# Optimization experiments

Hardware: AMD Instinct MI355X
Metric: run time of the kernel (lower is better)

## Reference

```python
import jax, jax.numpy as jnp
import numpy as np

EPS = 1e-4
# 8 box corners as min/max selection bits (matches the torch cat order:
# mmm, mmx, mxm, mxx, xmm, xmx, xxm, xxx)
_BITS = jnp.array([[0,0,0],[0,0,1],[0,1,0],[0,1,1],[1,0,0],[1,0,1],[1,1,0],[1,1,1]], dtype=jnp.float32)


def setup_inputs() -> dict:
    key = jax.random.key(0)
    k1, k2, k3, k4, k5 = jax.random.split(key, 5)
    K = 1024
    bb_min = jax.random.uniform(k1, (K, 3), minval=-1.0, maxval=1.0)
    size = jax.random.uniform(k2, (K, 3), minval=0.05, maxval=0.4)
    bb_max = bb_min + size
    # well-conditioned affine transforms: near-identity linear block + translation
    R = jnp.eye(3, dtype=jnp.float32) + 0.1 * jax.random.normal(k3, (K, 3, 3))
    t = 0.5 * jax.random.normal(k4, (K, 3))
    top = jnp.concatenate([R, t[:, :, None]], axis=-1)            # [K,3,4]
    bottom = jnp.broadcast_to(jnp.array([[0.0, 0.0, 0.0, 1.0]], dtype=jnp.float32), (K, 1, 4))
    abs_transforms = jnp.concatenate([top, bottom], axis=1)       # [K,4,4]
    selfpen_disable_mat = jax.random.randint(k5, (K, K), 0, 2) > 0
    return {"bb_min": bb_min, "bb_max": bb_max,
            "abs_transforms": abs_transforms,
            "selfpen_disable_mat": selfpen_disable_mat}


def reference(bb_min, bb_max, abs_transforms, selfpen_disable_mat):
    K = bb_min.shape[0]
    bits = _BITS.astype(bb_min.dtype)
    # corners: [K,8,3]
    corners = bb_min[:, None, :] * (1.0 - bits) + bb_max[:, None, :] * bits
    hcorners = jnp.concatenate([corners, jnp.ones((K, 8, 1), dtype=bb_min.dtype)], axis=-1)  # [K,8,4]
    # pose each box's corners by its own transform
    hposed = jnp.einsum('kij,kcj->kci', abs_transforms, hcorners)  # [K,8,4]
    # project every posed corner into every box's local frame
    back_trans = jnp.linalg.inv(abs_transforms)                    # [K,4,4]
    proj = jnp.einsum('kij,lcj->klci', back_trans, hposed)[..., :3]  # [K,K,8,3]
    inside = ((proj > bb_min[:, None, None, :] + EPS)
              & (proj < bb_max[:, None, None, :] - EPS)).all(axis=-1).any(axis=-1)  # [K,K]
    inside = inside & selfpen_disable_mat
    inside = inside | inside.T
    inside = jnp.tril(inside)
    # fixed-size index extraction (pad with -1): equivalent of
    # torch.stack(torch.where(inside)).sort(dim=0)[0].t()
    rows, cols = jnp.nonzero(inside, size=K * K, fill_value=-1)
    inds = jnp.stack([jnp.minimum(rows, cols), jnp.maximum(rows, cols)], axis=-1)  # [K*K,2], padded with -1
    return hposed[..., :3], inds
```

## Files before the change

kernel.cpp:

```cpp
#include <hip/hip_runtime.h>
#include <stdint.h>

#define KBOX 1024
#define EPSF 1e-4f
#define SLACK 3e-5f
#define ACT_TILES 2560
#define POSE_BLOCKS 4

#define BM_OFF 0
#define TC_OFF 131072

__device__ inline void inv_affine(const float r[12], float* o) {
    double m00 = r[0], m01 = r[1], m02 = r[2];
    double m10 = r[4], m11 = r[5], m12 = r[6];
    double m20 = r[8], m21 = r[9], m22 = r[10];
    double c00 = m11 * m22 - m12 * m21;
    double c01 = m12 * m20 - m10 * m22;
    double c02 = m10 * m21 - m11 * m20;
    double det = m00 * c00 + m01 * c01 + m02 * c02;
    double id = 1.0 / det;
    double i00 = c00 * id, i01 = (m02 * m21 - m01 * m22) * id, i02 = (m01 * m12 - m02 * m11) * id;
    double i10 = c01 * id, i11 = (m00 * m22 - m02 * m20) * id, i12 = (m02 * m10 - m00 * m12) * id;
    double i20 = c02 * id, i21 = (m01 * m20 - m00 * m21) * id, i22 = (m00 * m11 - m01 * m10) * id;
    double tx = r[3], ty = r[7], tz = r[11];
    o[0] = (float)i00; o[1] = (float)i01; o[2] = (float)i02;
    o[3] = (float)(-(i00 * tx + i01 * ty + i02 * tz));
    o[4] = (float)i10; o[5] = (float)i11; o[6] = (float)i12;
    o[7] = (float)(-(i10 * tx + i11 * ty + i12 * tz));
    o[8] = (float)i20; o[9] = (float)i21; o[10] = (float)i22;
    o[11] = (float)(-(i20 * tx + i21 * ty + i22 * tz));
}

__global__ void k_main(const float* __restrict__ bbmin, const float* __restrict__ bbmax,
                       const float* __restrict__ A, const uint8_t* __restrict__ disB,
                       float* __restrict__ out_hposed,
                       uint64_t* __restrict__ bm, uint32_t* __restrict__ tileCnt) {
    int bid = blockIdx.x;
    int t = threadIdx.x;

    if (bid >= ACT_TILES) {
        int k = (bid - ACT_TILES) * 256 + t;
        float r[12];
#pragma unroll
        for (int i = 0; i < 3; ++i) {
            float4 a4 = *(const float4*)(A + (size_t)k * 16 + i * 4);
            r[i * 4 + 0] = a4.x; r[i * 4 + 1] = a4.y; r[i * 4 + 2] = a4.z; r[i * 4 + 3] = a4.w;
        }
        float bmn[3], bmx[3];
#pragma unroll
        for (int i = 0; i < 3; ++i) { bmn[i] = bbmin[k * 3 + i]; bmx[i] = bbmax[k * 3 + i]; }
#pragma unroll
        for (int c = 0; c < 8; ++c) {
            float cx = ((c >> 2) & 1) ? bmx[0] : bmn[0];
            float cy = ((c >> 1) & 1) ? bmx[1] : bmn[1];
            float cz = (c & 1) ? bmx[2] : bmn[2];
#pragma unroll
            for (int i = 0; i < 3; ++i)
                out_hposed[(size_t)k * 24 + c * 3 + i] =
                    r[i * 4 + 0] * cx + r[i * 4 + 1] * cy + r[i * 4 + 2] * cz + r[i * 4 + 3];
        }
        return;
    }

    int k, j;
    if (bid < 256)       { k = bid;                      j = 0; }
    else if (bid < 768)  { k = 256 + ((bid - 256) >> 1); j = (bid - 256) & 1; }
    else if (bid < 1536) { k = 512 + (bid - 768) / 3;    j = (bid - 768) % 3; }
    else                 { k = 768 + ((bid - 1536) >> 2);j = (bid - 1536) & 3; }
    int lane = t & 63, wave = t >> 6;
    int l = j * 256 + t;

    uint32_t dw = ((const uint32_t*)disB)[lane];
    const bool isBool = __ballot((dw & 0xFFFFFF00u) != 0 ? 1 : 0) != 0ull;

    float rk[12];
#pragma unroll
    for (int i = 0; i < 3; ++i) {
        float4 a4 = *(const float4*)(A + (size_t)k * 16 + i * 4);
        rk[i * 4 + 0] = a4.x; rk[i * 4 + 1] = a4.y; rk[i * 4 + 2] = a4.z; rk[i * 4 + 3] = a4.w;
    }
    float bmnk[3], bmxk[3];
#pragma unroll
    for (int i = 0; i < 3; ++i) { bmnk[i] = bbmin[k * 3 + i]; bmxk[i] = bbmax[k * 3 + i]; }
    float wmnk[3], wmxk[3];
    {
        float cx = 0.5f * (bmnk[0] + bmxk[0]), hx = 0.5f * (bmxk[0] - bmnk[0]);
        float cy = 0.5f * (bmnk[1] + bmxk[1]), hy = 0.5f * (bmxk[1] - bmnk[1]);
        float cz = 0.5f * (bmnk[2] + bmxk[2]), hz = 0.5f * (bmxk[2] - bmnk[2]);
#pragma unroll
        for (int i = 0; i < 3; ++i) {
            float c = rk[i * 4 + 0] * cx + rk[i * 4 + 1] * cy + rk[i * 4 + 2] * cz + rk[i * 4 + 3];
            float h = fabsf(rk[i * 4 + 0]) * hx + fabsf(rk[i * 4 + 1]) * hy + fabsf(rk[i * 4 + 2]) * hz;
            wmnk[i] = c - h - SLACK;
            wmxk[i] = c + h + SLACK;
        }
    }

    float rl[12];
#pragma unroll
    for (int i = 0; i < 3; ++i) {
        float4 a4 = *(const float4*)(A + (size_t)l * 16 + i * 4);
        rl[i * 4 + 0] = a4.x; rl[i * 4 + 1] = a4.y; rl[i * 4 + 2] = a4.z; rl[i * 4 + 3] = a4.w;
    }
    float bmnl[3], bmxl[3];
#pragma unroll
    for (int i = 0; i < 3; ++i) { bmnl[i] = bbmin[l * 3 + i]; bmxl[i] = bbmax[l * 3 + i]; }
    float wcl[3], whl[3];
    {
        float cx = 0.5f * (bmnl[0] + bmxl[0]), hx = 0.5f * (bmxl[0] - bmnl[0]);
        float cy = 0.5f * (bmnl[1] + bmxl[1]), hy = 0.5f * (bmxl[1] - bmnl[1]);
        float cz = 0.5f * (bmnl[2] + bmxl[2]), hz = 0.5f * (bmxl[2] - bmnl[2]);
#pragma unroll
        for (int i = 0; i < 3; ++i) {
            wcl[i] = rl[i * 4 + 0] * cx + rl[i * 4 + 1] * cy + rl[i * 4 + 2] * cz + rl[i * 4 + 3];
            whl[i] = fabsf(rl[i * 4 + 0]) * hx + fabsf(rl[i * 4 + 1]) * hy + fabsf(rl[i * 4 + 2]) * hz;
        }
    }

    bool cand = false;
    if (l <= k) {
        cand = (wcl[0] - whl[0] <= wmxk[0]) & (wmnk[0] <= wcl[0] + whl[0]) &
               (wcl[1] - whl[1] <= wmxk[1]) & (wmnk[1] <= wcl[1] + whl[1]) &
               (wcl[2] - whl[2] <= wmxk[2]) & (wmnk[2] <= wcl[2] + whl[2]);
    }
    bool bit = false, dA = false, dB = false;
    if (cand) {
        if (isBool) {
            dA = disB[(size_t)k * KBOX + l] != 0;
            dB = disB[(size_t)l * KBOX + k] != 0;
        } else {
            const int* disI = (const int*)disB;
            dA = disI[(size_t)k * KBOX + l] != 0;
            dB = disI[(size_t)l * KBOX + k] != 0;
        }
    }
    if (cand && (dA | dB)) {
        if (dA) {
            float bk[12];
            inv_affine(rk, bk);
            bool rawA = false;
#pragma unroll
            for (int c = 0; c < 8; ++c) {
                float cx = ((c >> 2) & 1) ? bmxl[0] : bmnl[0];
                float cy = ((c >> 1) & 1) ? bmxl[1] : bmnl[1];
                float cz = (c & 1) ? bmxl[2] : bmnl[2];
                float px = rl[0] * cx + rl[1] * cy + rl[2] * cz + rl[3];
                float py = rl[4] * cx + rl[5] * cy + rl[6] * cz + rl[7];
                float pz = rl[8] * cx + rl[9] * cy + rl[10] * cz + rl[11];
                float x = bk[0] * px + bk[1] * py + bk[2] * pz + bk[3];
                float y = bk[4] * px + bk[5] * py + bk[6] * pz + bk[7];
                float z = bk[8] * px + bk[9] * py + bk[10] * pz + bk[11];
                rawA = rawA || (x > bmnk[0] + EPSF && x < bmxk[0] - EPSF &&
                                y > bmnk[1] + EPSF && y < bmxk[1] - EPSF &&
                                z > bmnk[2] + EPSF && z < bmxk[2] - EPSF);
            }
            bit = rawA;
        }
        if (dB && !bit) {
            float bl[12];
            inv_affine(rl, bl);
            bool rawB = false;
#pragma unroll
            for (int c = 0; c < 8; ++c) {
                float cx = ((c >> 2) & 1) ? bmxk[0] : bmnk[0];
                float cy = ((c >> 1) & 1) ? bmxk[1] : bmnk[1];
                float cz = (c & 1) ? bmxk[2] : bmnk[2];
                float px = rk[0] * cx + rk[1] * cy + rk[2] * cz + rk[3];
                float py = rk[4] * cx + rk[5] * cy + rk[6] * cz + rk[7];
                float pz = rk[8] * cx + rk[9] * cy + rk[10] * cz + rk[11];
                float x = bl[0] * px + bl[1] * py + bl[2] * pz + bl[3];
                float y = bl[4] * px + bl[5] * py + bl[6] * pz + bl[7];
                float z = bl[8] * px + bl[9] * py + bl[10] * pz + bl[11];
                rawB = rawB || (x > bmnl[0] + EPSF && x < bmxl[0] - EPSF &&
                                y > bmnl[1] + EPSF && y < bmxl[1] - EPSF &&
                                z > bmnl[2] + EPSF && z < bmxl[2] - EPSF);
            }
            bit = rawB;
        }
    }
    uint64_t word = __ballot(bit ? 1 : 0);
    __shared__ uint32_t wcnt[4];
    if (lane == 0) {
        bm[(size_t)k * 16 + j * 4 + wave] = word;
        wcnt[wave] = (uint32_t)__popcll(word);
    }
    __syncthreads();
    if (t == 0) tileCnt[(size_t)k * 4 + j] = wcnt[0] + wcnt[1] + wcnt[2] + wcnt[3];
}

__global__ void k_compact(const uint64_t* __restrict__ bm,
                          const uint32_t* __restrict__ tileCnt, float* __restrict__ out) {
    int b = blockIdx.x;
    int t = threadIdx.x;
    int wave = t >> 6, lane = t & 63;
    int k0 = 4 * b;
    __shared__ uint32_t baseW[4], totW[4], rowc[4];

    uint32_t sm = 0, st = 0;
#pragma unroll
    for (int rr = 0; rr < 4; ++rr) {
        int row = t + rr * 256;
        uint4 c4 = *(const uint4*)(tileCnt + (size_t)row * 4);
        uint32_t v = c4.x + ((row >= 256) ? c4.y : 0u) + ((row >= 512) ? c4.z : 0u) +
                     ((row >= 768) ? c4.w : 0u);
        sm += (row < k0) ? v : 0u;
        st += v;
    }
#pragma unroll
    for (int off = 32; off > 0; off >>= 1) { sm += __shfl_xor(sm, off); st += __shfl_xor(st, off); }
    if (lane == 0) { baseW[wave] = sm; totW[wave] = st; }
    if (t < 4) {
        int row = k0 + t;
        uint4 c4 = *(const uint4*)(tileCnt + (size_t)row * 4);
        rowc[t] = c4.x + ((row >= 256) ? c4.y : 0u) + ((row >= 512) ? c4.z : 0u) +
                  ((row >= 768) ? c4.w : 0u);
    }
    __syncthreads();
    uint32_t base = baseW[0] + baseW[1] + baseW[2] + baseW[3];
    uint32_t total = totW[0] + totW[1] + totW[2] + totW[3];

    float2* o2 = (float2*)out;
    for (uint32_t i = total + (uint32_t)b * 256 + t; i < (uint32_t)(KBOX * KBOX); i += 256 * 256)
        o2[i] = make_float2(-1.f, -1.f);

    uint32_t startw = base;
#pragma unroll
    for (int r = 0; r < 4; ++r)
        if (r < wave) startw += rowc[r];
    int k = k0 + wave;
    uint64_t w = (lane < 16 && lane * 64 <= k) ? bm[(size_t)k * 16 + lane] : 0ull;
    int c = (int)__popcll(w);
    int p = c;
#pragma unroll
    for (int off = 1; off < 64; off <<= 1) {
        int u = __shfl_up(p, off);
        if (lane >= off) p += u;
    }
    int ofs = (int)startw + (p - c);
    float fk = (float)k;
    while (w) {
        int bpos = __builtin_ctzll(w);
        int col = lane * 64 + bpos;
        out[2 * (size_t)ofs + 0] = (float)col;
        out[2 * (size_t)ofs + 1] = fk;
        ++ofs;
        w &= w - 1;
    }
}

extern "C" void kernel_launch(void* const* d_in, const int* in_sizes, int n_in,
                              void* d_out, int out_size, void* d_ws, size_t ws_size,
                              hipStream_t stream) {
    const float* bbmin = (const float*)d_in[0];
    const float* bbmax = (const float*)d_in[1];
    const float* A = (const float*)d_in[2];
    const uint8_t* dis = (const uint8_t*)d_in[3];
    float* out = (float*)d_out;

    char* ws = (char*)d_ws;
    uint64_t* bm = (uint64_t*)(ws + BM_OFF);
    uint32_t* tileCnt = (uint32_t*)(ws + TC_OFF);

    k_main<<<ACT_TILES + POSE_BLOCKS, 256, 0, stream>>>(
        bbmin, bbmax, A, dis, out, bm, tileCnt);
    k_compact<<<256, 256, 0, stream>>>(bm, tileCnt, out + KBOX * 24);
}
```

Measured before the change: 19.15 us.

## Process two k rows per block to reuse l-box data and halve block count

Each activity block now handles two consecutive k rows (k1, k1+1) for the same 256-wide l tile. The l-side transform, box bounds and world AABB are computed once and reused for both rows, and the number of activity blocks drops from 2560 to 1280. This cuts the repeated per-block setup and launch cost. The trade-off is less parallelism and a serial loop inside each block, and tiles where j*256 > k1 are skipped inside the loop rather than through the block mapping.

Result: slower. 20.68 us (+8.0%).

```diff
diff --git a/kernel.cpp b/kernel.cpp
--- a/kernel.cpp
+++ b/kernel.cpp
@@ -4,7 +4,7 @@
 #define KBOX 1024
 #define EPSF 1e-4f
 #define SLACK 3e-5f
-#define ACT_TILES 2560
+#define ACT_TILES 1280
 #define POSE_BLOCKS 4
 
 #define BM_OFF 0
@@ -62,39 +62,17 @@
         return;
     }
 
-    int k, j;
-    if (bid < 256)       { k = bid;                      j = 0; }
-    else if (bid < 768)  { k = 256 + ((bid - 256) >> 1); j = (bid - 256) & 1; }
-    else if (bid < 1536) { k = 512 + (bid - 768) / 3;    j = (bid - 768) % 3; }
-    else                 { k = 768 + ((bid - 1536) >> 2);j = (bid - 1536) & 3; }
+    int g, j;
+    if (bid < 128)       { g = bid;                       j = 0; }
+    else if (bid < 384)  { g = 128 + ((bid - 128) >> 1);  j = (bid - 128) & 1; }
+    else if (bid < 768)  { g = 256 + (bid - 384) / 3;     j = (bid - 384) % 3; }
+    else                 { g = 384 + ((bid - 768) >> 2);  j = (bid - 768) & 3; }
+    int k1 = 2 * g;
     int lane = t & 63, wave = t >> 6;
     int l = j * 256 + t;
 
-    uint32_t dw = ((const uint32_t*)disB)[lane];
-    const bool isBool = __ballot((dw & 0xFFFFFF00u) != 0 ? 1 : 0) != 0ull;
-
-    float rk[12];
-#pragma unroll
-    for (int i = 0; i < 3; ++i) {
-        float4 a4 = *(const float4*)(A + (size_t)k * 16 + i * 4);
-        rk[i * 4 + 0] = a4.x; rk[i * 4 + 1] = a4.y; rk[i * 4 + 2] = a4.z; rk[i * 4 + 3] = a4.w;
-    }
-    float bmnk[3], bmxk[3];
-#pragma unroll
-    for (int i = 0; i < 3; ++i) { bmnk[i] = bbmin[k * 3 + i]; bmxk[i] = bbmax[k * 3 + i]; }
-    float wmnk[3], wmxk[3];
-    {
-        float cx = 0.5f * (bmnk[0] + bmxk[0]), hx = 0.5f * (bmxk[0] - bmnk[0]);
-        float cy = 0.5f * (bmnk[1] + bmxk[1]), hy = 0.5f * (bmxk[1] - bmnk[1]);
-        float cz = 0.5f * (bmnk[2] + bmxk[2]), hz = 0.5f * (bmxk[2] - bmnk[2]);
-#pragma unroll
-        for (int i = 0; i < 3; ++i) {
-            float c = rk[i * 4 + 0] * cx + rk[i * 4 + 1] * cy + rk[i * 4 + 2] * cz + rk[i * 4 + 3];
-            float h = fabsf(rk[i * 4 + 0]) * hx + fabsf(rk[i * 4 + 1]) * hy + fabsf(rk[i * 4 + 2]) * hz;
-            wmnk[i] = c - h - SLACK;
-            wmxk[i] = c + h + SLACK;
-        }
-    }
+    uint32_t dwv = ((const uint32_t*)disB)[lane];
+    const bool isBool = __ballot((dwv & 0xFFFFFF00u) != 0 ? 1 : 0) != 0ull;
 
     float rl[12];
 #pragma unroll
@@ -117,75 +95,109 @@
         }
     }
 
-    bool cand = false;
-    if (l <= k) {
-        cand = (wcl[0] - whl[0] <= wmxk[0]) & (wmnk[0] <= wcl[0] + whl[0]) &
-               (wcl[1] - whl[1] <= wmxk[1]) & (wmnk[1] <= wcl[1] + whl[1]) &
-               (wcl[2] - whl[2] <= wmxk[2]) & (wmnk[2] <= wcl[2] + whl[2]);
-    }
-    bool bit = false, dA = false, dB = false;
-    if (cand) {
-        if (isBool) {
-            dA = disB[(size_t)k * KBOX + l] != 0;
-            dB = disB[(size_t)l * KBOX + k] != 0;
-        } else {
-            const int* disI = (const int*)disB;
-            dA = disI[(size_t)k * KBOX + l] != 0;
-            dB = disI[(size_t)l * KBOX + k] != 0;
-        }
-    }
-    if (cand && (dA | dB)) {
-        if (dA) {
-            float bk[12];
-            inv_affine(rk, bk);
-            bool rawA = false;
-#pragma unroll
-            for (int c = 0; c < 8; ++c) {
-                float cx = ((c >> 2) & 1) ? bmxl[0] : bmnl[0];
-                float cy = ((c >> 1) & 1) ? bmxl[1] : bmnl[1];
-                float cz = (c & 1) ? bmxl[2] : bmnl[2];
-                float px = rl[0] * cx + rl[1] * cy + rl[2] * cz + rl[3];
-                float py = rl[4] * cx + rl[5] * cy + rl[6] * cz + rl[7];
-                float pz = rl[8] * cx + rl[9] * cy + rl[10] * cz + rl[11];
-                float x = bk[0] * px + bk[1] * py + bk[2] * pz + bk[3];
-                float y = bk[4] * px + bk[5] * py + bk[6] * pz + bk[7];
-                float z = bk[8] * px + bk[9] * py + bk[10] * pz + bk[11];
-                rawA = rawA || (x > bmnk[0] + EPSF && x < bmxk[0] - EPSF &&
-                                y > bmnk[1] + EPSF && y < bmxk[1] - EPSF &&
-                                z > bmnk[2] + EPSF && z < bmxk[2] - EPSF);
-            }
-            bit = rawA;
-        }
-        if (dB && !bit) {
-            float bl[12];
-            inv_affine(rl, bl);
-            bool rawB = false;
-#pragma unroll
-            for (int c = 0; c < 8; ++c) {
-                float cx = ((c >> 2) & 1) ? bmxk[0] : bmnk[0];
-                float cy = ((c >> 1) & 1) ? bmxk[1] : bmnk[1];
-                float cz = (c & 1) ? bmxk[2] : bmnk[2];
-                float px = rk[0] * cx + rk[1] * cy + rk[2] * cz + rk[3];
-                float py = rk[4] * cx + rk[5] * cy + rk[6] * cz + rk[7];
-                float pz = rk[8] * cx + rk[9] * cy + rk[10] * cz + rk[11];
-                float x = bl[0] * px + bl[1] * py + bl[2] * pz + bl[3];
-                float y = bl[4] * px + bl[5] * py + bl[6] * pz + bl[7];
-                float z = bl[8] * px + bl[9] * py + bl[10] * pz + bl[11];
-                rawB = rawB || (x > bmnl[0] + EPSF && x < bmxl[0] - EPSF &&
-                                y > bmnl[1] + EPSF && y < bmxl[1] - EPSF &&
-                                z > bmnl[2] + EPSF && z < bmxl[2] - EPSF);
-            }
-            bit = rawB;
-        }
-    }
-    uint64_t word = __ballot(bit ? 1 : 0);
-    __shared__ uint32_t wcnt[4];
-    if (lane == 0) {
-        bm[(size_t)k * 16 + j * 4 + wave] = word;
-        wcnt[wave] = (uint32_t)__popcll(word);
+    __shared__ uint32_t wcnt[2][4];
+
+    for (int rr = 0; rr < 2; ++rr) {
+        int k = k1 + rr;
+        if (j * 256 > k) continue;
+
+        float rk[12];
+#pragma unroll
+        for (int i = 0; i < 3; ++i) {
+            float4 a4 = *(const float4*)(A + (size_t)k * 16 + i * 4);
+            rk[i * 4 + 0] = a4.x; rk[i * 4 + 1] = a4.y; rk[i * 4 + 2] = a4.z; rk[i * 4 + 3] = a4.w;
+        }
+        float bmnk[3], bmxk[3];
+#pragma unroll
+        for (int i = 0; i < 3; ++i) { bmnk[i] = bbmin[k * 3 + i]; bmxk[i] = bbmax[k * 3 + i]; }
+        float wmnk[3], wmxk[3];
+        {
+            float cx = 0.5f * (bmnk[0] + bmxk[0]), hx = 0.5f * (bmxk[0] - bmnk[0]);
+            float cy = 0.5f * (bmnk[1] + bmxk[1]), hy = 0.5f * (bmxk[1] - bmnk[1]);
+            float cz = 0.5f * (bmnk[2] + bmxk[2]), hz = 0.5f * (bmxk[2] - bmnk[2]);
+#pragma unroll
+            for (int i = 0; i < 3; ++i) {
+                float c = rk[i * 4 + 0] * cx + rk[i * 4 + 1] * cy + rk[i * 4 + 2] * cz + rk[i * 4 + 3];
+                float h = fabsf(rk[i * 4 + 0]) * hx + fabsf(rk[i * 4 + 1]) * hy +
+                          fabsf(rk[i * 4 + 2]) * hz;
+                wmnk[i] = c - h - SLACK;
+                wmxk[i] = c + h + SLACK;
+            }
+        }
+
+        bool cand = false;
+        if (l <= k) {
+            cand = (wcl[0] - whl[0] <= wmxk[0]) & (wmnk[0] <= wcl[0] + whl[0]) &
+                   (wcl[1] - whl[1] <= wmxk[1]) & (wmnk[1] <= wcl[1] + whl[1]) &
+                   (wcl[2] - whl[2] <= wmxk[2]) & (wmnk[2] <= wcl[2] + whl[2]);
+        }
+        bool bit = false, dA = false, dB = false;
+        if (cand) {
+            if (isBool) {
+                dA = disB[(size_t)k * KBOX + l] != 0;
+                dB = disB[(size_t)l * KBOX + k] != 0;
+            } else {
+                const int* disI = (const int*)disB;
+                dA = disI[(size_t)k * KBOX + l] != 0;
+                dB = disI[(size_t)l * KBOX + k] != 0;
+            }
+        }
+        if (cand && (dA | dB)) {
+            if (dA) {
+                float bk[12];
+                inv_affine(rk, bk);
+                bool rawA = false;
+#pragma unroll
+                for (int c = 0; c < 8; ++c) {
+                    float cx = ((c >> 2) & 1) ? bmxl[0] : bmnl[0];
+                    float cy = ((c >> 1) & 1) ? bmxl[1] : bmnl[1];
+                    float cz = (c & 1) ? bmxl[2] : bmnl[2];
+                    float px = rl[0] * cx + rl[1] * cy + rl[2] * cz + rl[3];
+                    float py = rl[4] * cx + rl[5] * cy + rl[6] * cz + rl[7];
+                    float pz = rl[8] * cx + rl[9] * cy + rl[10] * cz + rl[11];
+                    float x = bk[0] * px + bk[1] * py + bk[2] * pz + bk[3];
+                    float y = bk[4] * px + bk[5] * py + bk[6] * pz + bk[7];
+                    float z = bk[8] * px + bk[9] * py + bk[10] * pz + bk[11];
+                    rawA = rawA || (x > bmnk[0] + EPSF && x < bmxk[0] - EPSF &&
+                                    y > bmnk[1] + EPSF && y < bmxk[1] - EPSF &&
+                                    z > bmnk[2] + EPSF && z < bmxk[2] - EPSF);
+                }
+                bit = rawA;
+            }
+            if (dB && !bit) {
+                float bl[12];
+                inv_affine(rl, bl);
+                bool rawB = false;
+#pragma unroll
+                for (int c = 0; c < 8; ++c) {
+                    float cx = ((c >> 2) & 1) ? bmxk[0] : bmnk[0];
+                    float cy = ((c >> 1) & 1) ? bmxk[1] : bmnk[1];
+                    float cz = (c & 1) ? bmxk[2] : bmnk[2];
+                    float px = rk[0] * cx + rk[1] * cy + rk[2] * cz + rk[3];
+                    float py = rk[4] * cx + rk[5] * cy + rk[6] * cz + rk[7];
+                    float pz = rk[8] * cx + rk[9] * cy + rk[10] * cz + rk[11];
+                    float x = bl[0] * px + bl[1] * py + bl[2] * pz + bl[3];
+                    float y = bl[4] * px + bl[5] * py + bl[6] * pz + bl[7];
+                    float z = bl[8] * px + bl[9] * py + bl[10] * pz + bl[11];
+                    rawB = rawB || (x > bmnl[0] + EPSF && x < bmxl[0] - EPSF &&
+                                    y > bmnl[1] + EPSF && y < bmxl[1] - EPSF &&
+                                    z > bmnl[2] + EPSF && z < bmxl[2] - EPSF);
+                }
+                bit = rawB;
+            }
+        }
+        uint64_t word = __ballot(bit ? 1 : 0);
+        if (lane == 0) {
+            bm[(size_t)k * 16 + j * 4 + wave] = word;
+            wcnt[rr][wave] = (uint32_t)__popcll(word);
+        }
     }
     __syncthreads();
-    if (t == 0) tileCnt[(size_t)k * 4 + j] = wcnt[0] + wcnt[1] + wcnt[2] + wcnt[3];
+    if (t == 0) {
+        if (j * 256 <= k1)
+            tileCnt[(size_t)k1 * 4 + j] = wcnt[0][0] + wcnt[0][1] + wcnt[0][2] + wcnt[0][3];
+        tileCnt[(size_t)(k1 + 1) * 4 + j] = wcnt[1][0] + wcnt[1][1] + wcnt[1][2] + wcnt[1][3];
+    }
 }
 
 __global__ void k_compact(const uint64_t* __restrict__ bm,
```
